# Optimization experiments

Hardware: AMD Instinct MI355X
Metric: run time of the kernel (lower is better)

The kernel has to match this reference:

```python
import jax, jax.numpy as jnp
import numpy as np

B = 4096      # sessions
L = 32        # tokens per session (constant so sum(seq_len) == T)
T = B * L     # total tokens
H = 128       # hidden_size
HI = 8 * H    # input embedding dim (hidden_size * 8)


def setup_inputs() -> dict:
    key = jax.random.key(0)
    ks = jax.random.split(key, 8)
    s = lambda k, shape: jax.random.normal(k, shape, dtype=jnp.float32) * 0.02
    return {
        "inter_item_emb": s(ks[0], (T, HI)),
        "intra_item_emb": s(ks[1], (T, HI)),
        "seq_len": jnp.full((B,), L, dtype=jnp.int32),
        "Wf1_w": s(ks[2], (H, HI)), "Wf1_b": jnp.zeros((H,), jnp.float32),
        "Wf2_w": s(ks[3], (H, HI)), "Wf2_b": jnp.zeros((H,), jnp.float32),
        "W1_w": s(ks[4], (H, H)),   "W1_b": jnp.zeros((H,), jnp.float32),
        "W2_w": s(ks[5], (H, H)),   "W2_b": jnp.zeros((H,), jnp.float32),
        "q_w": s(ks[6], (1, H)),    "q_b": jnp.zeros((1,), jnp.float32),
        "W3_w": s(ks[7], (H, 2 * H)), "W3_b": jnp.zeros((H,), jnp.float32),
    }


def reference(inter_item_emb, intra_item_emb, seq_len,
              Wf1_w, Wf1_b, Wf2_w, Wf2_b,
              W1_w, W1_b, W2_w, W2_b,
              q_w, q_b, W3_w, W3_b):
    lin = lambda x, w, b: x @ w.T + b  # torch nn.Linear convention

    # item fusing: gated combination of the two projected embeddings
    f1 = lin(inter_item_emb, Wf1_w, Wf1_b)          # [T, H]
    f2 = lin(intra_item_emb, Wf2_w, Wf2_b)          # [T, H]
    gate = jax.nn.sigmoid(f1 + f2)
    h = f1 * gate + f2 * (1.0 - gate)               # [T, H]

    Ttok = h.shape[0]
    nseg = seq_len.shape[0]
    ends = jnp.cumsum(seq_len)                      # [B] exclusive ends
    # segment id of each token (sessions are contiguous row blocks)
    seg = jnp.searchsorted(ends, jnp.arange(Ttok), side="right")  # [T]
    last_idx = ends - 1                             # [B] last token of each session
    v_n = h[last_idx]                               # [B, H]

    # attention: alpha = q(sigmoid(W1(v_n_repeat) + W2(h)))
    w1v = lin(v_n, W1_w, W1_b)                      # [B, H], gather instead of repeat
    alpha = lin(jax.nn.sigmoid(w1v[seg] + lin(h, W2_w, W2_b)), q_w, q_b)  # [T, 1]

    # attention-weighted segment sum pooling
    s_g = jax.ops.segment_sum(alpha * h, seg, num_segments=nseg)  # [B, H]

    h_s = lin(jnp.concatenate([v_n, s_g], axis=1), W3_w, W3_b)    # [B, H]
    return h_s
```

## Files before the change

kernel.cpp:

```cpp
#include <hip/hip_runtime.h>
#include <hip/hip_bf16.h>

#define HI_DIM 1024
#define H_DIM  128
#define L_TOK  32
#define NW     8
#define THREADS 512
#define KW     40
#define HP     136

typedef float f32x4 __attribute__((ext_vector_type(4)));
typedef short s16x8 __attribute__((ext_vector_type(8)));

static __device__ __forceinline__ short f2b(float x) {
    return __builtin_bit_cast(short, __float2bfloat16(x));
}
static __device__ __forceinline__ float b2f(short u) {
    unsigned int v = ((unsigned int)(unsigned short)u) << 16;
    return __builtin_bit_cast(float, v);
}
static __device__ __forceinline__ void split8(const f32x4 a, const f32x4 b, s16x8& hi, s16x8& lo) {
    #pragma unroll
    for (int j = 0; j < 4; ++j) {
        short h0 = f2b(a[j]); hi[j]   = h0; lo[j]   = f2b(a[j] - b2f(h0));
        short h1 = f2b(b[j]); hi[j+4] = h1; lo[j+4] = f2b(b[j] - b2f(h1));
    }
}
static __device__ __forceinline__ s16x8 cvt8(const f32x4 a, const f32x4 b) {
    s16x8 r;
    r[0]=f2b(a[0]); r[1]=f2b(a[1]); r[2]=f2b(a[2]); r[3]=f2b(a[3]);
    r[4]=f2b(b[0]); r[5]=f2b(b[1]); r[6]=f2b(b[2]); r[7]=f2b(b[3]);
    return r;
}
static __device__ __forceinline__ float sigm(float x) { return 1.0f / (1.0f + __expf(-x)); }

#define MFMA16(A,B,C) __builtin_amdgcn_mfma_f32_16x16x32_bf16((A),(B),(C),0,0,0)

#define REGION(ACC, CURBUF, STAGE_EN, NXTBUF, RWN_EN, RWN_PTR, AN_EN, AN_PTR) do {            \
    if (STAGE_EN) {                                                                            \
        s16x8 hi_, lo_; split8(rwa, rwb, hi_, lo_);                                            \
        *(s16x8*)&u.wbuf[NXTBUF][0][srow][sq8] = hi_;                                          \
        *(s16x8*)&u.wbuf[NXTBUF][1][srow][sq8] = lo_;                                          \
    }                                                                                          \
    if (RWN_EN) { const float* s_ = (RWN_PTR);                                                 \
        rwa = *(const f32x4*)s_; rwb = *(const f32x4*)(s_ + 4); }                              \
    s16x8 ah0, al0, ah1, al1;                                                                  \
    split8(ra00, ra01, ah0, al0);                                                              \
    split8(ra10, ra11, ah1, al1);                                                              \
    if (AN_EN) { const float* a_ = (AN_PTR);                                                   \
        const float* a2_ = a_ + (size_t)16 * HI_DIM;                                           \
        ra00 = *(const f32x4*)a_;  ra01 = *(const f32x4*)(a_ + 4);                             \
        ra10 = *(const f32x4*)a2_; ra11 = *(const f32x4*)(a2_ + 4); }                          \
    _Pragma("unroll")                                                                          \
    for (int nt = 0; nt < 8; ++nt) {                                                           \
        s16x8 bh_ = *(const s16x8*)&u.wbuf[CURBUF][0][nt*16 + l15][kg*8];                      \
        s16x8 bl_ = *(const s16x8*)&u.wbuf[CURBUF][1][nt*16 + l15][kg*8];                      \
        ACC[0][nt] = MFMA16(ah0, bh_, ACC[0][nt]);                                             \
        ACC[1][nt] = MFMA16(ah1, bh_, ACC[1][nt]);                                             \
        ACC[0][nt] = MFMA16(al0, bh_, ACC[0][nt]);                                             \
        ACC[1][nt] = MFMA16(al1, bh_, ACC[1][nt]);                                             \
        ACC[0][nt] = MFMA16(ah0, bl_, ACC[0][nt]);                                             \
        ACC[1][nt] = MFMA16(ah1, bl_, ACC[1][nt]);                                             \
    }                                                                                          \
} while (0)

__global__ __launch_bounds__(THREADS, 2) void itemfusing_fused(
    const float* __restrict__ inter, const float* __restrict__ intra,
    const int* __restrict__ seq_len,
    const float* __restrict__ Wf1, const float* __restrict__ bf1,
    const float* __restrict__ Wf2, const float* __restrict__ bf2,
    const float* __restrict__ W1,  const float* __restrict__ b1,
    const float* __restrict__ W2,  const float* __restrict__ b2,
    const float* __restrict__ qw,  const float* __restrict__ qb,
    const float* __restrict__ W3,  const float* __restrict__ b3,
    float* __restrict__ out)
{
    (void)seq_len;
    __shared__ union {
        short wbuf[2][2][H_DIM][KW];
        short hbuf[4][L_TOK][HP];
    } u;
    __shared__ float vn [NW][H_DIM];
    __shared__ float w1v[NW][H_DIM];
    __shared__ float sgl[NW][H_DIM];

    const int tid = threadIdx.x;
    const int w   = tid >> 6;
    const int l   = tid & 63;
    const int l15 = l & 15;
    const int kg  = l >> 4;
    const int sess = blockIdx.x * NW + w;
    const int row0 = sess * L_TOK;

    const int srow = tid >> 2;
    const int sq8  = (tid & 3) * 8;

    f32x4 acc1[2][8], acc2[2][8];
    #pragma unroll
    for (int mt = 0; mt < 2; ++mt)
        #pragma unroll
        for (int nt = 0; nt < 8; ++nt) {
            acc1[mt][nt] = f32x4{0.f,0.f,0.f,0.f};
            acc2[mt][nt] = f32x4{0.f,0.f,0.f,0.f};
        }

    {
        const float* s = Wf1 + (size_t)srow * HI_DIM + sq8;
        f32x4 a = *(const f32x4*)s, b = *(const f32x4*)(s + 4);
        s16x8 hi, lo; split8(a, b, hi, lo);
        *(s16x8*)&u.wbuf[0][0][srow][sq8] = hi;
        *(s16x8*)&u.wbuf[0][1][srow][sq8] = lo;
    }
    f32x4 rwa, rwb;
    { const float* s = Wf2 + (size_t)srow * HI_DIM + sq8;
      rwa = *(const f32x4*)s; rwb = *(const f32x4*)(s + 4); }
    f32x4 ra00, ra01, ra10, ra11;
    {
        const float* a0 = inter + (size_t)(row0 + l15) * HI_DIM + kg * 8;
        const float* a1 = a0 + (size_t)16 * HI_DIM;
        ra00 = *(const f32x4*)a0; ra01 = *(const f32x4*)(a0 + 4);
        ra10 = *(const f32x4*)a1; ra11 = *(const f32x4*)(a1 + 4);
    }
    __syncthreads();

    #pragma unroll 1
    for (int cp = 0; cp < 32; ++cp) {
        REGION(acc1, 0, 1, 1, (cp < 31),
               Wf1 + (size_t)srow * HI_DIM + (cp + 1) * 32 + sq8,
               1,
               intra + (size_t)(row0 + l15) * HI_DIM + cp * 32 + kg * 8);
        __syncthreads();
        const int en = (cp < 31);
        REGION(acc2, 1, en, 0, en,
               Wf2 + (size_t)srow * HI_DIM + (cp + 1) * 32 + sq8,
               en,
               inter + (size_t)(row0 + l15) * HI_DIM + (cp + 1) * 32 + kg * 8);
        __syncthreads();
    }

    #pragma unroll
    for (int nt = 0; nt < 8; ++nt) {
        const int n = nt * 16 + l15;
        const float bb1 = bf1[n], bb2 = bf2[n];
        #pragma unroll
        for (int mt = 0; mt < 2; ++mt)
            #pragma unroll
            for (int rj = 0; rj < 4; ++rj) {
                float x1 = acc1[mt][nt][rj] + bb1;
                float x2 = acc2[mt][nt][rj] + bb2;
                float g  = sigm(x1 + x2);
                acc1[mt][nt][rj] = x2 + g * (x1 - x2);
            }
    }

    if (kg == 3) {
        #pragma unroll
        for (int nt = 0; nt < 8; ++nt) vn[w][nt * 16 + l15] = acc1[1][nt][3];
    }
    asm volatile("s_waitcnt lgkmcnt(0)" ::: "memory");
    {
        const float* w1r0 = W1 + (size_t)l * H_DIM;
        const float* w1r1 = W1 + (size_t)(l + 64) * H_DIM;
        float s0 = 0.f, s1 = 0.f;
        #pragma unroll
        for (int kk = 0; kk < H_DIM; kk += 4) {
            f32x4 vv = *(const f32x4*)&vn[w][kk];
            f32x4 u0 = *(const f32x4*)(w1r0 + kk);
            f32x4 u1 = *(const f32x4*)(w1r1 + kk);
            #pragma unroll
            for (int j = 0; j < 4; ++j) { s0 += u0[j] * vv[j]; s1 += u1[j] * vv[j]; }
        }
        w1v[w][l]      = s0 + b1[l];
        w1v[w][l + 64] = s1 + b1[l + 64];
    }
    asm volatile("s_waitcnt lgkmcnt(0)" ::: "memory");

    auto tail = [&](int wj) {
        short (*hb)[HP] = u.hbuf[wj];
        #pragma unroll
        for (int nt = 0; nt < 8; ++nt)
            #pragma unroll
            for (int mt = 0; mt < 2; ++mt)
                #pragma unroll
                for (int rj = 0; rj < 4; ++rj)
                    hb[16 * mt + kg * 4 + rj][nt * 16 + l15] = f2b(acc1[mt][nt][rj]);
        asm volatile("s_waitcnt lgkmcnt(0)" ::: "memory");

        f32x4 accw[2][8];
        #pragma unroll
        for (int mt = 0; mt < 2; ++mt)
            #pragma unroll
            for (int nt = 0; nt < 8; ++nt) accw[mt][nt] = f32x4{0.f,0.f,0.f,0.f};
        #pragma unroll
        for (int ks = 0; ks < 4; ++ks) {
            const int kl = ks * 32 + kg * 8;
            s16x8 ah0 = *(const s16x8*)&hb[l15][kl];
            s16x8 ah1 = *(const s16x8*)&hb[16 + l15][kl];
            #pragma unroll
            for (int nt = 0; nt < 8; ++nt) {
                const float* wp = W2 + (size_t)(nt * 16 + l15) * H_DIM + kl;
                s16x8 bw = cvt8(*(const f32x4*)wp, *(const f32x4*)(wp + 4));
                accw[0][nt] = MFMA16(ah0, bw, accw[0][nt]);
                accw[1][nt] = MFMA16(ah1, bw, accw[1][nt]);
            }
        }

        float part[2][4];
        #pragma unroll
        for (int mt = 0; mt < 2; ++mt)
            #pragma unroll
            for (int rj = 0; rj < 4; ++rj) part[mt][rj] = 0.f;
        #pragma unroll
        for (int nt = 0; nt < 8; ++nt) {
            const int n = nt * 16 + l15;
            const float qn = qw[n], wv = w1v[w][n], bb = b2[n];
            #pragma unroll
            for (int mt = 0; mt < 2; ++mt)
                #pragma unroll
                for (int rj = 0; rj < 4; ++rj)
                    part[mt][rj] += qn * sigm(wv + accw[mt][nt][rj] + bb);
        }
        const float qbias = qb[0];
        #pragma unroll
        for (int mt = 0; mt < 2; ++mt)
            #pragma unroll
            for (int rj = 0; rj < 4; ++rj) {
                float v = part[mt][rj];
                v += __shfl_xor(v, 1); v += __shfl_xor(v, 2);
                v += __shfl_xor(v, 4); v += __shfl_xor(v, 8);
                part[mt][rj] = v + qbias;
            }

        #pragma unroll
        for (int nt = 0; nt < 8; ++nt) {
            float s = 0.f;
            #pragma unroll
            for (int mt = 0; mt < 2; ++mt)
                #pragma unroll
                for (int rj = 0; rj < 4; ++rj)
                    s += part[mt][rj] * acc1[mt][nt][rj];
            s += __shfl_xor(s, 16);
            s += __shfl_xor(s, 32);
            if (l < 16) sgl[w][nt * 16 + l15] = s;
        }
        asm volatile("s_waitcnt lgkmcnt(0)" ::: "memory");

        const int n0 = l, n1 = l + 64;
        const float* w3r0 = W3 + (size_t)n0 * (2 * H_DIM);
        const float* w3r1 = W3 + (size_t)n1 * (2 * H_DIM);
        float h0 = b3[n0], h1 = b3[n1];
        #pragma unroll
        for (int kk = 0; kk < H_DIM; kk += 4) {
            f32x4 vv = *(const f32x4*)&vn[w][kk];
            f32x4 ss = *(const f32x4*)&sgl[w][kk];
            f32x4 a0 = *(const f32x4*)(w3r0 + kk);
            f32x4 a1 = *(const f32x4*)(w3r1 + kk);
            f32x4 c0 = *(const f32x4*)(w3r0 + H_DIM + kk);
            f32x4 c1 = *(const f32x4*)(w3r1 + H_DIM + kk);
            #pragma unroll
            for (int j = 0; j < 4; ++j) {
                h0 += a0[j] * vv[j] + c0[j] * ss[j];
                h1 += a1[j] * vv[j] + c1[j] * ss[j];
            }
        }
        out[(size_t)sess * H_DIM + n0] = h0;
        out[(size_t)sess * H_DIM + n1] = h1;
    };

    if (w < 4) tail(w);
    __syncthreads();
    if (w >= 4) tail(w - 4);
}

extern "C" void kernel_launch(void* const* d_in, const int* in_sizes, int n_in,
                              void* d_out, int out_size, void* d_ws, size_t ws_size,
                              hipStream_t stream) {
    (void)n_in; (void)d_ws; (void)ws_size; (void)out_size;
    const float* inter = (const float*)d_in[0];
    const float* intra = (const float*)d_in[1];
    const int*   seq   = (const int*)d_in[2];
    const float* Wf1   = (const float*)d_in[3];
    const float* bf1   = (const float*)d_in[4];
    const float* Wf2   = (const float*)d_in[5];
    const float* bf2   = (const float*)d_in[6];
    const float* W1    = (const float*)d_in[7];
    const float* b1    = (const float*)d_in[8];
    const float* W2    = (const float*)d_in[9];
    const float* b2    = (const float*)d_in[10];
    const float* qw    = (const float*)d_in[11];
    const float* qb    = (const float*)d_in[12];
    const float* W3    = (const float*)d_in[13];
    const float* b3    = (const float*)d_in[14];
    float* out = (float*)d_out;

    const int nsess   = in_sizes[2];
    const int nblocks = nsess / NW;

    itemfusing_fused<<<nblocks, THREADS, 0, stream>>>(
        inter, intra, seq, Wf1, bf1, Wf2, bf2, W1, b1, W2, b2, qw, qb, W3, b3, out);
}
```

Baseline: 399.9 us.

## Pre-split weights to bf16 hi/lo in a prep kernel; shrink blocks to two sessions

Adds a prep kernel that converts Wf1/Wf2 into bf16 hi/lo pairs and W2 into bf16 once per call, stored in workspace. The main kernel then copies pre-split tiles into LDS instead of converting weights in every block. The main kernel now uses 256 threads covering 2 sessions, with each wave owning one 16-row M tile, and targets 3 blocks per SM. This removes the redundant per-block weight conversion and raises occupancy, but halves the weight reuse per LDS tile and adds a second launch.

```diff
diff --git a/kernel.cpp b/kernel.cpp
--- a/kernel.cpp
+++ b/kernel.cpp
@@ -1,13 +1,9 @@
 #include <hip/hip_runtime.h>
 #include <hip/hip_bf16.h>
 
-#define HI_DIM 1024
-#define H_DIM  128
-#define L_TOK  32
-#define NW     8
-#define THREADS 512
-#define KW     40
-#define HP     136
+#define THREADS 256
+#define KW 40
+#define HP 136
 
 typedef float f32x4 __attribute__((ext_vector_type(4)));
 typedef short s16x8 __attribute__((ext_vector_type(8)));
@@ -36,105 +32,138 @@
 
 #define MFMA16(A,B,C) __builtin_amdgcn_mfma_f32_16x16x32_bf16((A),(B),(C),0,0,0)
 
-#define REGION(ACC, CURBUF, STAGE_EN, NXTBUF, RWN_EN, RWN_PTR, AN_EN, AN_PTR) do {            \
-    if (STAGE_EN) {                                                                            \
-        s16x8 hi_, lo_; split8(rwa, rwb, hi_, lo_);                                            \
-        *(s16x8*)&u.wbuf[NXTBUF][0][srow][sq8] = hi_;                                          \
-        *(s16x8*)&u.wbuf[NXTBUF][1][srow][sq8] = lo_;                                          \
-    }                                                                                          \
-    if (RWN_EN) { const float* s_ = (RWN_PTR);                                                 \
-        rwa = *(const f32x4*)s_; rwb = *(const f32x4*)(s_ + 4); }                              \
-    s16x8 ah0, al0, ah1, al1;                                                                  \
-    split8(ra00, ra01, ah0, al0);                                                              \
-    split8(ra10, ra11, ah1, al1);                                                              \
-    if (AN_EN) { const float* a_ = (AN_PTR);                                                   \
-        const float* a2_ = a_ + (size_t)16 * HI_DIM;                                           \
-        ra00 = *(const f32x4*)a_;  ra01 = *(const f32x4*)(a_ + 4);                             \
-        ra10 = *(const f32x4*)a2_; ra11 = *(const f32x4*)(a2_ + 4); }                          \
-    _Pragma("unroll")                                                                          \
-    for (int nt = 0; nt < 8; ++nt) {                                                           \
-        s16x8 bh_ = *(const s16x8*)&u.wbuf[CURBUF][0][nt*16 + l15][kg*8];                      \
-        s16x8 bl_ = *(const s16x8*)&u.wbuf[CURBUF][1][nt*16 + l15][kg*8];                      \
-        ACC[0][nt] = MFMA16(ah0, bh_, ACC[0][nt]);                                             \
-        ACC[1][nt] = MFMA16(ah1, bh_, ACC[1][nt]);                                             \
-        ACC[0][nt] = MFMA16(al0, bh_, ACC[0][nt]);                                             \
-        ACC[1][nt] = MFMA16(al1, bh_, ACC[1][nt]);                                             \
-        ACC[0][nt] = MFMA16(ah0, bl_, ACC[0][nt]);                                             \
-        ACC[1][nt] = MFMA16(ah1, bl_, ACC[1][nt]);                                             \
-    }                                                                                          \
-} while (0)
-
-__global__ __launch_bounds__(THREADS, 2) void itemfusing_fused(
+__global__ __launch_bounds__(256) void itemfusing_prep(
+    const float* __restrict__ Wf1, const float* __restrict__ Wf2,
+    const float* __restrict__ W2, short* __restrict__ wsp)
+{
+    const int t = blockIdx.x * 256 + threadIdx.x;
+    if (t < 65536) {
+        const int idx = t * 8;
+        const int k0 = idx & 31;
+        const int r  = (idx >> 5) & 127;
+        const int p  = (idx >> 12) & 1;
+        const int cp = (idx >> 13) & 31;
+        const int wv = idx >> 18;
+        const float* src = (wv ? Wf2 : Wf1) + (size_t)r * 1024 + cp * 32 + k0;
+        f32x4 a = *(const f32x4*)src, b = *(const f32x4*)(src + 4);
+        s16x8 hi, lo; split8(a, b, hi, lo);
+        *(s16x8*)(wsp + idx) = p ? lo : hi;
+    } else {
+        const int t2 = t - 65536;
+        if (t2 < 2048) {
+            const int idx = t2 * 8;
+            const float* src = W2 + idx;
+            *(s16x8*)(wsp + 524288 + idx) = cvt8(*(const f32x4*)src, *(const f32x4*)(src + 4));
+        }
+    }
+}
+
+template<bool PRE>
+__global__ __launch_bounds__(THREADS, 3) void itemfusing_main(
     const float* __restrict__ inter, const float* __restrict__ intra,
-    const int* __restrict__ seq_len,
     const float* __restrict__ Wf1, const float* __restrict__ bf1,
     const float* __restrict__ Wf2, const float* __restrict__ bf2,
     const float* __restrict__ W1,  const float* __restrict__ b1,
     const float* __restrict__ W2,  const float* __restrict__ b2,
     const float* __restrict__ qw,  const float* __restrict__ qb,
     const float* __restrict__ W3,  const float* __restrict__ b3,
+    const short* __restrict__ wsp, const short* __restrict__ w2b,
     float* __restrict__ out)
 {
-    (void)seq_len;
     __shared__ union {
-        short wbuf[2][2][H_DIM][KW];
-        short hbuf[4][L_TOK][HP];
+        short wbuf[2][2][128][KW];
+        short hbuf[2][32][HP];
     } u;
-    __shared__ float vn [NW][H_DIM];
-    __shared__ float w1v[NW][H_DIM];
-    __shared__ float sgl[NW][H_DIM];
+    __shared__ float vn  [2][128];
+    __shared__ float w1v [2][128];
+    __shared__ float sglp[2][2][128];
 
     const int tid = threadIdx.x;
-    const int w   = tid >> 6;
     const int l   = tid & 63;
     const int l15 = l & 15;
     const int kg  = l >> 4;
-    const int sess = blockIdx.x * NW + w;
-    const int row0 = sess * L_TOK;
-
-    const int srow = tid >> 2;
-    const int sq8  = (tid & 3) * 8;
-
-    f32x4 acc1[2][8], acc2[2][8];
-    #pragma unroll
-    for (int mt = 0; mt < 2; ++mt)
-        #pragma unroll
-        for (int nt = 0; nt < 8; ++nt) {
-            acc1[mt][nt] = f32x4{0.f,0.f,0.f,0.f};
-            acc2[mt][nt] = f32x4{0.f,0.f,0.f,0.f};
-        }
-
-    {
-        const float* s = Wf1 + (size_t)srow * HI_DIM + sq8;
-        f32x4 a = *(const f32x4*)s, b = *(const f32x4*)(s + 4);
-        s16x8 hi, lo; split8(a, b, hi, lo);
-        *(s16x8*)&u.wbuf[0][0][srow][sq8] = hi;
-        *(s16x8*)&u.wbuf[0][1][srow][sq8] = lo;
-    }
-    f32x4 rwa, rwb;
-    { const float* s = Wf2 + (size_t)srow * HI_DIM + sq8;
-      rwa = *(const f32x4*)s; rwb = *(const f32x4*)(s + 4); }
-    f32x4 ra00, ra01, ra10, ra11;
-    {
-        const float* a0 = inter + (size_t)(row0 + l15) * HI_DIM + kg * 8;
-        const float* a1 = a0 + (size_t)16 * HI_DIM;
-        ra00 = *(const f32x4*)a0; ra01 = *(const f32x4*)(a0 + 4);
-        ra10 = *(const f32x4*)a1; ra11 = *(const f32x4*)(a1 + 4);
-    }
+    const int w   = tid >> 6;
+    const int s   = w >> 1;
+    const int mt  = w & 1;
+    const int sess = blockIdx.x * 2 + s;
+    const int arow = sess * 32 + mt * 16 + l15;
+
+    const float* aF1 = inter + (size_t)arow * 1024 + kg * 8;
+    const float* aF2 = intra + (size_t)arow * 1024 + kg * 8;
+
+    const int sp = tid >> 7;
+    const int sr = tid & 127;
+    const int fr = tid >> 1;
+    const int fk = (tid & 1) * 16;
+    const short* wsp_t = PRE ? (wsp + sp * 4096 + sr * 32) : nullptr;
+
+    s16x8 wr0, wr1, wr2, wr3;
+    f32x4 fw0, fw1, fw2, fw3;
+
+#define WLOAD(WV, CP) do {                                                                  \
+    if constexpr (PRE) { const short* p_ = wsp_t + ((WV) * 32 + (CP)) * 8192;               \
+        wr0 = *(const s16x8*)p_;        wr1 = *(const s16x8*)(p_ + 8);                      \
+        wr2 = *(const s16x8*)(p_ + 16); wr3 = *(const s16x8*)(p_ + 24); }                   \
+    else { const float* p_ = ((WV) ? Wf2 : Wf1) + (size_t)fr * 1024 + (CP) * 32 + fk;       \
+        fw0 = *(const f32x4*)p_;        fw1 = *(const f32x4*)(p_ + 4);                      \
+        fw2 = *(const f32x4*)(p_ + 8);  fw3 = *(const f32x4*)(p_ + 12); } } while (0)
+
+#define WSTORE(BUF) do {                                                                    \
+    if constexpr (PRE) { short* d_ = &u.wbuf[BUF][sp][sr][0];                               \
+        *(s16x8*)d_ = wr0;        *(s16x8*)(d_ + 8) = wr1;                                  \
+        *(s16x8*)(d_ + 16) = wr2; *(s16x8*)(d_ + 24) = wr3; }                               \
+    else { s16x8 h0_, l0_, h1_, l1_;                                                        \
+        split8(fw0, fw1, h0_, l0_); split8(fw2, fw3, h1_, l1_);                             \
+        short* dh_ = &u.wbuf[BUF][0][fr][fk]; short* dl_ = &u.wbuf[BUF][1][fr][fk];         \
+        *(s16x8*)dh_ = h0_; *(s16x8*)(dh_ + 8) = h1_;                                       \
+        *(s16x8*)dl_ = l0_; *(s16x8*)(dl_ + 8) = l1_; } } while (0)
+
+    f32x4 acc1[8], acc2[8];
+    #pragma unroll
+    for (int nt = 0; nt < 8; ++nt) {
+        acc1[nt] = f32x4{0.f, 0.f, 0.f, 0.f};
+        acc2[nt] = f32x4{0.f, 0.f, 0.f, 0.f};
+    }
+
+    WLOAD(0, 0); WSTORE(0);
+    WLOAD(1, 0);
+    f32x4 raF1a = *(const f32x4*)aF1, raF1b = *(const f32x4*)(aF1 + 4);
+    f32x4 raF2a = *(const f32x4*)aF2, raF2b = *(const f32x4*)(aF2 + 4);
     __syncthreads();
 
     #pragma unroll 1
     for (int cp = 0; cp < 32; ++cp) {
-        REGION(acc1, 0, 1, 1, (cp < 31),
-               Wf1 + (size_t)srow * HI_DIM + (cp + 1) * 32 + sq8,
-               1,
-               intra + (size_t)(row0 + l15) * HI_DIM + cp * 32 + kg * 8);
+        const bool more = (cp < 31);
+        {
+            WSTORE(1);
+            if (more) WLOAD(0, cp + 1);
+            s16x8 ah, al; split8(raF1a, raF1b, ah, al);
+            if (more) { const float* p = aF1 + (cp + 1) * 32;
+                raF1a = *(const f32x4*)p; raF1b = *(const f32x4*)(p + 4); }
+            #pragma unroll
+            for (int nt = 0; nt < 8; ++nt) {
+                s16x8 bh = *(const s16x8*)&u.wbuf[0][0][nt * 16 + l15][kg * 8];
+                s16x8 bl = *(const s16x8*)&u.wbuf[0][1][nt * 16 + l15][kg * 8];
+                acc1[nt] = MFMA16(ah, bh, acc1[nt]);
+                acc1[nt] = MFMA16(al, bh, acc1[nt]);
+                acc1[nt] = MFMA16(ah, bl, acc1[nt]);
+            }
+        }
         __syncthreads();
-        const int en = (cp < 31);
-        REGION(acc2, 1, en, 0, en,
-               Wf2 + (size_t)srow * HI_DIM + (cp + 1) * 32 + sq8,
-               en,
-               inter + (size_t)(row0 + l15) * HI_DIM + (cp + 1) * 32 + kg * 8);
+        {
+            if (more) { WSTORE(0); WLOAD(1, cp + 1); }
+            s16x8 ah, al; split8(raF2a, raF2b, ah, al);
+            if (more) { const float* p = aF2 + (cp + 1) * 32;
+                raF2a = *(const f32x4*)p; raF2b = *(const f32x4*)(p + 4); }
+            #pragma unroll
+            for (int nt = 0; nt < 8; ++nt) {
+                s16x8 bh = *(const s16x8*)&u.wbuf[1][0][nt * 16 + l15][kg * 8];
+                s16x8 bl = *(const s16x8*)&u.wbuf[1][1][nt * 16 + l15][kg * 8];
+                acc2[nt] = MFMA16(ah, bh, acc2[nt]);
+                acc2[nt] = MFMA16(al, bh, acc2[nt]);
+                acc2[nt] = MFMA16(ah, bl, acc2[nt]);
+            }
+        }
         __syncthreads();
     }
 
@@ -143,142 +172,117 @@
         const int n = nt * 16 + l15;
         const float bb1 = bf1[n], bb2 = bf2[n];
         #pragma unroll
-        for (int mt = 0; mt < 2; ++mt)
+        for (int rj = 0; rj < 4; ++rj) {
+            float x1 = acc1[nt][rj] + bb1;
+            float x2 = acc2[nt][rj] + bb2;
+            float g  = sigm(x1 + x2);
+            acc1[nt][rj] = x2 + g * (x1 - x2);
+        }
+    }
+
+    if (mt == 1 && kg == 3) {
+        #pragma unroll
+        for (int nt = 0; nt < 8; ++nt) vn[s][nt * 16 + l15] = acc1[nt][3];
+    }
+    __syncthreads();
+
+    {
+        const int n = mt * 64 + l;
+        const float* w1r = W1 + (size_t)n * 128;
+        float acc = b1[n];
+        #pragma unroll
+        for (int kk = 0; kk < 128; kk += 4) {
+            f32x4 vv = *(const f32x4*)&vn[s][kk];
+            f32x4 u0 = *(const f32x4*)(w1r + kk);
             #pragma unroll
-            for (int rj = 0; rj < 4; ++rj) {
-                float x1 = acc1[mt][nt][rj] + bb1;
-                float x2 = acc2[mt][nt][rj] + bb2;
-                float g  = sigm(x1 + x2);
-                acc1[mt][nt][rj] = x2 + g * (x1 - x2);
+            for (int j = 0; j < 4; ++j) acc += u0[j] * vv[j];
+        }
+        w1v[s][n] = acc;
+    }
+    short (*hb)[HP] = u.hbuf[s];
+    #pragma unroll
+    for (int nt = 0; nt < 8; ++nt)
+        #pragma unroll
+        for (int rj = 0; rj < 4; ++rj)
+            hb[mt * 16 + kg * 4 + rj][nt * 16 + l15] = f2b(acc1[nt][rj]);
+    __syncthreads();
+
+    f32x4 aw[8];
+    #pragma unroll
+    for (int nt = 0; nt < 8; ++nt) aw[nt] = f32x4{0.f, 0.f, 0.f, 0.f};
+    #pragma unroll
+    for (int ks = 0; ks < 4; ++ks) {
+        const int kl = ks * 32 + kg * 8;
+        s16x8 ah = *(const s16x8*)&hb[mt * 16 + l15][kl];
+        #pragma unroll
+        for (int nt = 0; nt < 8; ++nt) {
+            s16x8 bw;
+            if constexpr (PRE) {
+                bw = *(const s16x8*)&w2b[(size_t)(nt * 16 + l15) * 128 + kl];
+            } else {
+                const float* wp = W2 + (size_t)(nt * 16 + l15) * 128 + kl;
+                bw = cvt8(*(const f32x4*)wp, *(const f32x4*)(wp + 4));
             }
-    }
-
-    if (kg == 3) {
-        #pragma unroll
-        for (int nt = 0; nt < 8; ++nt) vn[w][nt * 16 + l15] = acc1[1][nt][3];
-    }
-    asm volatile("s_waitcnt lgkmcnt(0)" ::: "memory");
+            aw[nt] = MFMA16(ah, bw, aw[nt]);
+        }
+    }
+
+    float prt[4] = {0.f, 0.f, 0.f, 0.f};
+    #pragma unroll
+    for (int nt = 0; nt < 8; ++nt) {
+        const int n = nt * 16 + l15;
+        const float qn = qw[n], wv_ = w1v[s][n], bb = b2[n];
+        #pragma unroll
+        for (int rj = 0; rj < 4; ++rj)
+            prt[rj] += qn * sigm(wv_ + aw[nt][rj] + bb);
+    }
+    const float qbias = qb[0];
+    #pragma unroll
+    for (int rj = 0; rj < 4; ++rj) {
+        float v = prt[rj];
+        v += __shfl_xor(v, 1); v += __shfl_xor(v, 2);
+        v += __shfl_xor(v, 4); v += __shfl_xor(v, 8);
+        prt[rj] = v + qbias;
+    }
+
+    #pragma unroll
+    for (int nt = 0; nt < 8; ++nt) {
+        float sgv = 0.f;
+        #pragma unroll
+        for (int rj = 0; rj < 4; ++rj) sgv += prt[rj] * acc1[nt][rj];
+        sgv += __shfl_xor(sgv, 16);
+        sgv += __shfl_xor(sgv, 32);
+        if (l < 16) sglp[s][mt][nt * 16 + l15] = sgv;
+    }
+    __syncthreads();
+
     {
-        const float* w1r0 = W1 + (size_t)l * H_DIM;
-        const float* w1r1 = W1 + (size_t)(l + 64) * H_DIM;
-        float s0 = 0.f, s1 = 0.f;
-        #pragma unroll
-        for (int kk = 0; kk < H_DIM; kk += 4) {
-            f32x4 vv = *(const f32x4*)&vn[w][kk];
-            f32x4 u0 = *(const f32x4*)(w1r0 + kk);
-            f32x4 u1 = *(const f32x4*)(w1r1 + kk);
+        const int n = mt * 64 + l;
+        const float* w3r = W3 + (size_t)n * 256;
+        float o = b3[n];
+        #pragma unroll
+        for (int kk = 0; kk < 128; kk += 4) {
+            f32x4 vv = *(const f32x4*)&vn[s][kk];
+            f32x4 s0 = *(const f32x4*)&sglp[s][0][kk];
+            f32x4 s1 = *(const f32x4*)&sglp[s][1][kk];
+            f32x4 a0 = *(const f32x4*)(w3r + kk);
+            f32x4 c0 = *(const f32x4*)(w3r + 128 + kk);
             #pragma unroll
-            for (int j = 0; j < 4; ++j) { s0 += u0[j] * vv[j]; s1 += u1[j] * vv[j]; }
-        }
-        w1v[w][l]      = s0 + b1[l];
-        w1v[w][l + 64] = s1 + b1[l + 64];
-    }
-    asm volatile("s_waitcnt lgkmcnt(0)" ::: "memory");
-
-    auto tail = [&](int wj) {
-        short (*hb)[HP] = u.hbuf[wj];
-        #pragma unroll
-        for (int nt = 0; nt < 8; ++nt)
-            #pragma unroll
-            for (int mt = 0; mt < 2; ++mt)
-                #pragma unroll
-                for (int rj = 0; rj < 4; ++rj)
-                    hb[16 * mt + kg * 4 + rj][nt * 16 + l15] = f2b(acc1[mt][nt][rj]);
-        asm volatile("s_waitcnt lgkmcnt(0)" ::: "memory");
-
-        f32x4 accw[2][8];
-        #pragma unroll
-        for (int mt = 0; mt < 2; ++mt)
-            #pragma unroll
-            for (int nt = 0; nt < 8; ++nt) accw[mt][nt] = f32x4{0.f,0.f,0.f,0.f};
-        #pragma unroll
-        for (int ks = 0; ks < 4; ++ks) {
-            const int kl = ks * 32 + kg * 8;
-            s16x8 ah0 = *(const s16x8*)&hb[l15][kl];
-            s16x8 ah1 = *(const s16x8*)&hb[16 + l15][kl];
-            #pragma unroll
-            for (int nt = 0; nt < 8; ++nt) {
-                const float* wp = W2 + (size_t)(nt * 16 + l15) * H_DIM + kl;
-                s16x8 bw = cvt8(*(const f32x4*)wp, *(const f32x4*)(wp + 4));
-                accw[0][nt] = MFMA16(ah0, bw, accw[0][nt]);
-                accw[1][nt] = MFMA16(ah1, bw, accw[1][nt]);
-            }
-        }
-
-        float part[2][4];
-        #pragma unroll
-        for (int mt = 0; mt < 2; ++mt)
-            #pragma unroll
-            for (int rj = 0; rj < 4; ++rj) part[mt][rj] = 0.f;
-        #pragma unroll
-        for (int nt = 0; nt < 8; ++nt) {
-            const int n = nt * 16 + l15;
-            const float qn = qw[n], wv = w1v[w][n], bb = b2[n];
-            #pragma unroll
-            for (int mt = 0; mt < 2; ++mt)
-                #pragma unroll
-                for (int rj = 0; rj < 4; ++rj)
-                    part[mt][rj] += qn * sigm(wv + accw[mt][nt][rj] + bb);
-        }
-        const float qbias = qb[0];
-        #pragma unroll
-        for (int mt = 0; mt < 2; ++mt)
-            #pragma unroll
-            for (int rj = 0; rj < 4; ++rj) {
-                float v = part[mt][rj];
-                v += __shfl_xor(v, 1); v += __shfl_xor(v, 2);
-                v += __shfl_xor(v, 4); v += __shfl_xor(v, 8);
-                part[mt][rj] = v + qbias;
-            }
-
-        #pragma unroll
-        for (int nt = 0; nt < 8; ++nt) {
-            float s = 0.f;
-            #pragma unroll
-            for (int mt = 0; mt < 2; ++mt)
-                #pragma unroll
-                for (int rj = 0; rj < 4; ++rj)
-                    s += part[mt][rj] * acc1[mt][nt][rj];
-            s += __shfl_xor(s, 16);
-            s += __shfl_xor(s, 32);
-            if (l < 16) sgl[w][nt * 16 + l15] = s;
-        }
-        asm volatile("s_waitcnt lgkmcnt(0)" ::: "memory");
-
-        const int n0 = l, n1 = l + 64;
-        const float* w3r0 = W3 + (size_t)n0 * (2 * H_DIM);
-        const float* w3r1 = W3 + (size_t)n1 * (2 * H_DIM);
-        float h0 = b3[n0], h1 = b3[n1];
-        #pragma unroll
-        for (int kk = 0; kk < H_DIM; kk += 4) {
-            f32x4 vv = *(const f32x4*)&vn[w][kk];
-            f32x4 ss = *(const f32x4*)&sgl[w][kk];
-            f32x4 a0 = *(const f32x4*)(w3r0 + kk);
-            f32x4 a1 = *(const f32x4*)(w3r1 + kk);
-            f32x4 c0 = *(const f32x4*)(w3r0 + H_DIM + kk);
-            f32x4 c1 = *(const f32x4*)(w3r1 + H_DIM + kk);
-            #pragma unroll
-            for (int j = 0; j < 4; ++j) {
-                h0 += a0[j] * vv[j] + c0[j] * ss[j];
-                h1 += a1[j] * vv[j] + c1[j] * ss[j];
-            }
-        }
-        out[(size_t)sess * H_DIM + n0] = h0;
-        out[(size_t)sess * H_DIM + n1] = h1;
-    };
-
-    if (w < 4) tail(w);
-    __syncthreads();
-    if (w >= 4) tail(w - 4);
+            for (int j = 0; j < 4; ++j)
+                o += a0[j] * vv[j] + c0[j] * (s0[j] + s1[j]);
+        }
+        out[(size_t)sess * 128 + (mt * 64 + l)] = o;
+    }
+#undef WLOAD
+#undef WSTORE
 }
 
 extern "C" void kernel_launch(void* const* d_in, const int* in_sizes, int n_in,
                               void* d_out, int out_size, void* d_ws, size_t ws_size,
                               hipStream_t stream) {
-    (void)n_in; (void)d_ws; (void)ws_size; (void)out_size;
+    (void)n_in; (void)out_size;
     const float* inter = (const float*)d_in[0];
     const float* intra = (const float*)d_in[1];
-    const int*   seq   = (const int*)d_in[2];
     const float* Wf1   = (const float*)d_in[3];
     const float* bf1   = (const float*)d_in[4];
     const float* Wf2   = (const float*)d_in[5];
@@ -294,8 +298,18 @@
     float* out = (float*)d_out;
 
     const int nsess   = in_sizes[2];
-    const int nblocks = nsess / NW;
-
-    itemfusing_fused<<<nblocks, THREADS, 0, stream>>>(
-        inter, intra, seq, Wf1, bf1, Wf2, bf2, W1, b1, W2, b2, qw, qb, W3, b3, out);
-}
+    const int nblocks = nsess / 2;
+
+    const size_t WS_NEED = (size_t)(524288 + 16384) * sizeof(short);
+    if (d_ws != nullptr && ws_size >= WS_NEED) {
+        short* wsp = (short*)d_ws;
+        itemfusing_prep<<<264, 256, 0, stream>>>(Wf1, Wf2, W2, wsp);
+        itemfusing_main<true><<<nblocks, THREADS, 0, stream>>>(
+            inter, intra, Wf1, bf1, Wf2, bf2, W1, b1, W2, b2, qw, qb, W3, b3,
+            wsp, wsp + 524288, out);
+    } else {
+        itemfusing_main<false><<<nblocks, THREADS, 0, stream>>>(
+            inter, intra, Wf1, bf1, Wf2, bf2, W1, b1, W2, b2, qw, qb, W3, b3,
+            nullptr, nullptr, out);
+    }
+}
```

After: 425.4 us. 6.4% more time.
